# Kernel tuning notes

Measured on AMD Instinct MI355X. Metric: run time of the kernel, lower is better.

Reference implementation:

```python
import jax, jax.numpy as jnp
import numpy as np

N = 4096
RANK = 4
B = 2048
DT = 1.0
TAU = 1.0
ALPHA = float(np.sqrt(np.pi) / 2.0)  # erf slope so phi'(0)=1


def setup_inputs() -> dict:
    key = jax.random.key(0)
    k1, k2, k3, k4, k5, k6 = jax.random.split(key, 6)
    return {
        "x_t": jax.random.normal(k1, (1, B), dtype=jnp.float32),
        "h": jax.random.normal(k2, (N, B), dtype=jnp.float32),
        "m": jax.random.normal(k3, (N, 1), dtype=jnp.float32),
        "u": jax.random.normal(k4, (N, RANK), dtype=jnp.float32),
        "v": jax.random.normal(k5, (N, RANK), dtype=jnp.float32),
        "z": jax.random.normal(k6, (N, 1), dtype=jnp.float32),
    }


def reference(x_t, h, m, u, v, z):
    # phi(h) = erf(alpha * h)
    phi_h = jax.lax.erf(ALPHA * h)                      # [N, B]
    # W @ phi_h with W = (1/N) u v^T, reassociated to exploit low rank
    # (mathematically identical to materializing W)
    wph = (u @ (v.T @ phi_h)) / N                       # [N, B]
    h_update = wph + m @ x_t                            # [N, B]
    h_new = h + (DT / TAU) * (-h + h_update)            # [N, B]
    y = (z.T @ phi_h) / N                               # [1, B]
    return (y, h_new)
```

## Files before the change

kernel.cpp:

```cpp
#include <hip/hip_runtime.h>
#include <math.h>

#define N 4096
#define B 2048
#define RANK 4
#define ALPHA 0.8862269254527580f
#define INV_N (1.0f / 4096.0f)

#define RPB1 16
#define SPLITS (N / RPB1)
#define P (5 * B)
#define CH 8
#define SPC (SPLITS / CH)
#define RPB3 4

typedef float vf4 __attribute__((ext_vector_type(4)));

__global__ __launch_bounds__(512) void k_reduce_partial(
    const float* __restrict__ h, const float* __restrict__ v,
    const float* __restrict__ z, float* __restrict__ partials) {
  __shared__ float lv[RPB1 * RANK];
  __shared__ float lz[RPB1];
  const int tid = threadIdx.x;
  const int row0 = blockIdx.x * RPB1;

  if (tid < RPB1 * RANK) {
    lv[tid] = v[row0 * RANK + tid];
  } else if (tid < RPB1 * RANK + RPB1) {
    lz[tid - RPB1 * RANK] = z[row0 + (tid - RPB1 * RANK)];
  }
  __syncthreads();

  vf4 a0 = {0.f, 0.f, 0.f, 0.f};
  vf4 a1 = a0, a2 = a0, a3 = a0, a4 = a0;

  const float* hp = h + (size_t)row0 * B + tid * 4;
#pragma unroll
  for (int r = 0; r < RPB1; ++r) {
    const vf4 hv =
        __builtin_nontemporal_load((const vf4*)(hp + (size_t)r * B));
    vf4 p;
    p.x = erff(ALPHA * hv.x);
    p.y = erff(ALPHA * hv.y);
    p.z = erff(ALPHA * hv.z);
    p.w = erff(ALPHA * hv.w);
    const float v0 = lv[r * 4 + 0], v1 = lv[r * 4 + 1];
    const float v2 = lv[r * 4 + 2], v3 = lv[r * 4 + 3];
    const float zr = lz[r];
    a0.x = fmaf(v0, p.x, a0.x); a0.y = fmaf(v0, p.y, a0.y);
    a0.z = fmaf(v0, p.z, a0.z); a0.w = fmaf(v0, p.w, a0.w);
    a1.x = fmaf(v1, p.x, a1.x); a1.y = fmaf(v1, p.y, a1.y);
    a1.z = fmaf(v1, p.z, a1.z); a1.w = fmaf(v1, p.w, a1.w);
    a2.x = fmaf(v2, p.x, a2.x); a2.y = fmaf(v2, p.y, a2.y);
    a2.z = fmaf(v2, p.z, a2.z); a2.w = fmaf(v2, p.w, a2.w);
    a3.x = fmaf(v3, p.x, a3.x); a3.y = fmaf(v3, p.y, a3.y);
    a3.z = fmaf(v3, p.z, a3.z); a3.w = fmaf(v3, p.w, a3.w);
    a4.x = fmaf(zr, p.x, a4.x); a4.y = fmaf(zr, p.y, a4.y);
    a4.z = fmaf(zr, p.z, a4.z); a4.w = fmaf(zr, p.w, a4.w);
  }

  float* pp = partials + (size_t)blockIdx.x * P + tid * 4;
  *(vf4*)(pp + 0 * B) = a0;
  *(vf4*)(pp + 1 * B) = a1;
  *(vf4*)(pp + 2 * B) = a2;
  *(vf4*)(pp + 3 * B) = a3;
  *(vf4*)(pp + 4 * B) = a4;
}

__global__ __launch_bounds__(256) void k_reduce_a(
    const float* __restrict__ partials, float* __restrict__ partial2) {
  const int f = blockIdx.x * 256 + threadIdx.x;
  const int j = blockIdx.y;
  const float* pp = partials + (size_t)(j * SPC) * P + f;
  float s = 0.f;
#pragma unroll 8
  for (int sp = 0; sp < SPC; ++sp)
    s += pp[(size_t)sp * P];
  partial2[(size_t)j * P + f] = s;
}

__global__ __launch_bounds__(256) void k_reduce_b(
    const float* __restrict__ partial2, float* __restrict__ sfin,
    float* __restrict__ y) {
  const int f = blockIdx.x * 256 + threadIdx.x;
  float s = 0.f;
#pragma unroll
  for (int j = 0; j < CH; ++j)
    s += partial2[(size_t)j * P + f];
  if (f < RANK * B)
    sfin[f] = s;
  else
    y[f - RANK * B] = s * INV_N;
}

__global__ __launch_bounds__(256) void k_update(
    const float* __restrict__ sfin, const float* __restrict__ u,
    const float* __restrict__ m, const float* __restrict__ x,
    float* __restrict__ hnew) {
  const int tid = threadIdx.x;
  const int row0 = blockIdx.x * RPB3;
  const int c0 = tid * 4;

  const vf4 sA0 = *(const vf4*)(sfin + 0 * B + c0);
  const vf4 sA1 = *(const vf4*)(sfin + 1 * B + c0);
  const vf4 sA2 = *(const vf4*)(sfin + 2 * B + c0);
  const vf4 sA3 = *(const vf4*)(sfin + 3 * B + c0);
  const vf4 xa  = *(const vf4*)(x + c0);
  const vf4 sB0 = *(const vf4*)(sfin + 0 * B + c0 + 1024);
  const vf4 sB1 = *(const vf4*)(sfin + 1 * B + c0 + 1024);
  const vf4 sB2 = *(const vf4*)(sfin + 2 * B + c0 + 1024);
  const vf4 sB3 = *(const vf4*)(sfin + 3 * B + c0 + 1024);
  const vf4 xb  = *(const vf4*)(x + c0 + 1024);

  float* op = hnew + (size_t)row0 * B + c0;
#pragma unroll
  for (int i = 0; i < RPB3; ++i) {
    const int n = row0 + i;
    const vf4 uv = *(const vf4*)(u + (size_t)n * RANK);
    const float mv = m[n];
    vf4 oA, oB;
    oA.x = fmaf(mv, xa.x,
                (sA0.x * uv.x + sA1.x * uv.y + sA2.x * uv.z + sA3.x * uv.w) * INV_N);
    oA.y = fmaf(mv, xa.y,
                (sA0.y * uv.x + sA1.y * uv.y + sA2.y * uv.z + sA3.y * uv.w) * INV_N);
    oA.z = fmaf(mv, xa.z,
                (sA0.z * uv.x + sA1.z * uv.y + sA2.z * uv.z + sA3.z * uv.w) * INV_N);
    oA.w = fmaf(mv, xa.w,
                (sA0.w * uv.x + sA1.w * uv.y + sA2.w * uv.z + sA3.w * uv.w) * INV_N);
    oB.x = fmaf(mv, xb.x,
                (sB0.x * uv.x + sB1.x * uv.y + sB2.x * uv.z + sB3.x * uv.w) * INV_N);
    oB.y = fmaf(mv, xb.y,
                (sB0.y * uv.x + sB1.y * uv.y + sB2.y * uv.z + sB3.y * uv.w) * INV_N);
    oB.z = fmaf(mv, xb.z,
                (sB0.z * uv.x + sB1.z * uv.y + sB2.z * uv.z + sB3.z * uv.w) * INV_N);
    oB.w = fmaf(mv, xb.w,
                (sB0.w * uv.x + sB1.w * uv.y + sB2.w * uv.z + sB3.w * uv.w) * INV_N);
    __builtin_nontemporal_store(oA, (vf4*)(op + (size_t)i * B));
    __builtin_nontemporal_store(oB, (vf4*)(op + (size_t)i * B + 1024));
  }
}

extern "C" void kernel_launch(void* const* d_in, const int* in_sizes, int n_in,
                              void* d_out, int out_size, void* d_ws,
                              size_t ws_size, hipStream_t stream) {
  const float* x = (const float*)d_in[0];
  const float* h = (const float*)d_in[1];
  const float* m = (const float*)d_in[2];
  const float* u = (const float*)d_in[3];
  const float* v = (const float*)d_in[4];
  const float* z = (const float*)d_in[5];

  float* y = (float*)d_out;
  float* hnew = (float*)d_out + B;

  float* partials = (float*)d_ws;
  float* partial2 = partials + (size_t)SPLITS * P;
  float* sfin = partial2 + (size_t)CH * P;

  k_reduce_partial<<<SPLITS, 512, 0, stream>>>(h, v, z, partials);
  k_reduce_a<<<dim3(P / 256, CH), 256, 0, stream>>>(partials, partial2);
  k_reduce_b<<<P / 256, 256, 0, stream>>>(partial2, sfin, y);
  k_update<<<N / RPB3, 256, 0, stream>>>(sfin, u, m, x, hnew);
}
```

Measured before the change: 116.8 us.

## Fuse two-stage partial reduction into one kernel and halve rows per block

Replaces the two-step global reduction (k_reduce_a then k_reduce_b, through an intermediate buffer) with one kernel. Each block handles a 64-column stripe, eight thread groups sum strided partials, and the groups are combined in shared memory. Rows per block in the first pass drop from 16 to 8, doubling the block count and the partials buffer. The nontemporal hint on h loads is removed. This saves a launch and the intermediate round trip, but adds partials traffic and gives the final reduction only 160 blocks.

```diff
diff --git a/kernel.cpp b/kernel.cpp
--- a/kernel.cpp
+++ b/kernel.cpp
@@ -7,11 +7,12 @@
 #define ALPHA 0.8862269254527580f
 #define INV_N (1.0f / 4096.0f)
 
-#define RPB1 16
+#define RPB1 8
 #define SPLITS (N / RPB1)
 #define P (5 * B)
-#define CH 8
-#define SPC (SPLITS / CH)
+#define STRIPE 64
+#define GRP 8
+#define SPG (SPLITS / GRP)
 #define RPB3 4
 
 typedef float vf4 __attribute__((ext_vector_type(4)));
@@ -37,8 +38,7 @@
   const float* hp = h + (size_t)row0 * B + tid * 4;
 #pragma unroll
   for (int r = 0; r < RPB1; ++r) {
-    const vf4 hv =
-        __builtin_nontemporal_load((const vf4*)(hp + (size_t)r * B));
+    const vf4 hv = *(const vf4*)(hp + (size_t)r * B);
     vf4 p;
     p.x = erff(ALPHA * hv.x);
     p.y = erff(ALPHA * hv.y);
@@ -67,30 +67,31 @@
   *(vf4*)(pp + 4 * B) = a4;
 }
 
-__global__ __launch_bounds__(256) void k_reduce_a(
-    const float* __restrict__ partials, float* __restrict__ partial2) {
-  const int f = blockIdx.x * 256 + threadIdx.x;
-  const int j = blockIdx.y;
-  const float* pp = partials + (size_t)(j * SPC) * P + f;
-  float s = 0.f;
+__global__ __launch_bounds__(512) void k_reduce_final(
+    const float* __restrict__ partials, float* __restrict__ sfin,
+    float* __restrict__ y) {
+  __shared__ float red[GRP][STRIPE];
+  const int c = threadIdx.x & (STRIPE - 1);
+  const int g = threadIdx.x >> 6;
+  const int f0 = blockIdx.x * STRIPE;
+  const float* pp = partials + (size_t)(g * SPG) * P + f0 + c;
+  float ssum = 0.f;
 #pragma unroll 8
-  for (int sp = 0; sp < SPC; ++sp)
-    s += pp[(size_t)sp * P];
-  partial2[(size_t)j * P + f] = s;
-}
-
-__global__ __launch_bounds__(256) void k_reduce_b(
-    const float* __restrict__ partial2, float* __restrict__ sfin,
-    float* __restrict__ y) {
-  const int f = blockIdx.x * 256 + threadIdx.x;
-  float s = 0.f;
+  for (int sp = 0; sp < SPG; ++sp)
+    ssum += pp[(size_t)sp * P];
+  red[g][c] = ssum;
+  __syncthreads();
+  if (threadIdx.x < STRIPE) {
+    float tot = 0.f;
 #pragma unroll
-  for (int j = 0; j < CH; ++j)
-    s += partial2[(size_t)j * P + f];
-  if (f < RANK * B)
-    sfin[f] = s;
-  else
-    y[f - RANK * B] = s * INV_N;
+    for (int g2 = 0; g2 < GRP; ++g2)
+      tot += red[g2][threadIdx.x];
+    const int f = f0 + threadIdx.x;
+    if (f < RANK * B)
+      sfin[f] = tot;
+    else
+      y[f - RANK * B] = tot * INV_N;
+  }
 }
 
 __global__ __launch_bounds__(256) void k_update(
@@ -154,11 +155,9 @@
   float* hnew = (float*)d_out + B;
 
   float* partials = (float*)d_ws;
-  float* partial2 = partials + (size_t)SPLITS * P;
-  float* sfin = partial2 + (size_t)CH * P;
+  float* sfin = partials + (size_t)SPLITS * P;
 
   k_reduce_partial<<<SPLITS, 512, 0, stream>>>(h, v, z, partials);
-  k_reduce_a<<<dim3(P / 256, CH), 256, 0, stream>>>(partials, partial2);
-  k_reduce_b<<<P / 256, 256, 0, stream>>>(partial2, sfin, y);
+  k_reduce_final<<<P / STRIPE, 512, 0, stream>>>(partials, sfin, y);
   k_update<<<N / RPB3, 256, 0, stream>>>(sfin, u, m, x, hnew);
 }
```

Result: faster. 107.8 us (-7.7%).
